# Kernel tuning notes

Measured on AMD Instinct MI355X. Metric: run time of the kernel, lower is better.

## Reference

```python
import jax, jax.numpy as jnp
import numpy as np
from jax import lax

SPATIAL = 4
PAD = 1
STRIDE = 1


def _route(x, rconv_w, rconv_b, fc_w, fc_b, num_experts):
    # x: (b, c, h, w); adaptive avg pool to (SPATIAL, SPATIAL) -- h,w divisible by SPATIAL
    b, c, h, w = x.shape
    pooled = x.reshape(b, c, SPATIAL, h // SPATIAL, SPATIAL, w // SPATIAL).mean(axis=(3, 5))
    # 1x1 conv: (b,c,s,s) x (rc,c) -> (b,rc,s,s)
    y = jnp.einsum('bcij,rc->brij', pooled, rconv_w) + rconv_b[None, :, None, None]
    y = jax.nn.relu(y).reshape(b, -1)                      # (b, rc*s*s)
    y = jax.nn.relu(y @ fc_w.T + fc_b)                     # (b, num_experts*c)
    y = y.reshape(b, num_experts, c)
    return jax.nn.sigmoid(y)                               # (b, k, c)


def _conv_per_sample(xi, wi):
    # xi: (c_in, h, w), wi: (c_out, c_in, kh, kw)
    out = lax.conv_general_dilated(
        xi[None], wi, window_strides=(STRIDE, STRIDE),
        padding=[(PAD, PAD), (PAD, PAD)],
        dimension_numbers=('NCHW', 'OIHW', 'NCHW'))
    return out[0]


def setup_inputs() -> dict:
    key = jax.random.key(0)
    ks = jax.random.split(key, 6)
    b, c_in, c_out, kk, ne = 16, 256, 256, 3, 3
    rc = max(c_in // 16, 16)  # reduction_channels = 16
    x = jax.random.normal(ks[0], (b, c_in, 64, 64), dtype=jnp.float32)
    expert_weight = jax.random.normal(ks[1], (ne, c_out, c_in, kk, kk), dtype=jnp.float32) * 0.02
    rconv_w = jax.random.normal(ks[2], (rc, c_in), dtype=jnp.float32) * 0.05
    rconv_b = jax.random.normal(ks[3], (rc,), dtype=jnp.float32) * 0.05
    fc_w = jax.random.normal(ks[4], (ne * c_in, rc * SPATIAL * SPATIAL), dtype=jnp.float32) * 0.05
    fc_b = jax.random.normal(ks[5], (ne * c_in,), dtype=jnp.float32) * 0.05
    return {"x": x, "expert_weight": expert_weight, "rconv_w": rconv_w,
            "rconv_b": rconv_b, "fc_w": fc_w, "fc_b": fc_b}


def reference(x, expert_weight, rconv_w, rconv_b, fc_w, fc_b):
    ne = expert_weight.shape[0]
    r = _route(x, rconv_w, rconv_b, fc_w, fc_b, ne)        # (b, k, c_in)
    # per-sample combined weights: routing scales input channels of each expert kernel
    w = jnp.einsum('bkc,kocij->bocij', r, expert_weight)    # (b, c_out, c_in, kh, kw)
    out = jax.vmap(_conv_per_sample)(x, w)                  # (b, c_out, h', w')
    return out
```

## Files before the change

kernel.cpp:

```cpp
#include <hip/hip_runtime.h>

#define B_   16
#define C_   256
#define OC_  256
#define H_   64
#define W_   64

typedef __attribute__((ext_vector_type(8)))  __bf16 bf16x8;
typedef __attribute__((ext_vector_type(4)))  float  f32x4;
typedef __attribute__((ext_vector_type(16))) float  f32x16;

__device__ __forceinline__ short f2bf(float f) {
    unsigned u = __float_as_uint(f);
    u += 0x7fffu + ((u >> 16) & 1u);
    return (short)(u >> 16);
}
__device__ __forceinline__ unsigned pk2(float a, float b) {
    return (unsigned(f2bf(a)) & 0xffffu) | (unsigned(f2bf(b)) << 16);
}
__device__ __forceinline__ void gll16(const void* g, void* l) {
    __builtin_amdgcn_global_load_lds(
        (const __attribute__((address_space(1))) unsigned int*)g,
        (__attribute__((address_space(3))) unsigned int*)l,
        16, 0, 0);
}

__global__ __launch_bounds__(256) void k_transpose_pool(
        const float* __restrict__ x, short* __restrict__ xt, float* __restrict__ pooled) {
    int y = blockIdx.x, b = blockIdx.y, t = threadIdx.x;
    int si = y >> 4;
    int lane = t & 63, wv = t >> 6;
    int xq = lane & 15, cw = lane >> 4;
    __shared__ float tile[64 * 67];

    for (int cc = 0; cc < 4; ++cc) {
        int cbase = cc * 64;
        if (cc) __syncthreads();
        #pragma unroll
        for (int r = 0; r < 4; ++r) {
            int c_l = r * 16 + wv * 4 + cw;
            float4 v = *(const float4*)&x[(((size_t)b * C_ + cbase + c_l) * H_ + y) * W_ + xq * 4];
            float* tp = &tile[c_l * 67 + xq * 4];
            tp[0] = v.x; tp[1] = v.y; tp[2] = v.z; tp[3] = v.w;
            float s = v.x + v.y + v.z + v.w;
            s += __shfl_xor(s, 1);
            s += __shfl_xor(s, 2);
            if ((lane & 3) == 0)
                atomicAdd(&pooled[((b * 4 + si) * 4 + (xq >> 2)) * 256 + cbase + c_l], s);
        }
        __syncthreads();
        #pragma unroll
        for (int r2 = 0; r2 < 2; ++r2) {
            int u = r2 * 256 + t;
            int xx = u >> 3, cgl = u & 7;
            float f[8];
            #pragma unroll
            for (int j = 0; j < 8; ++j) f[j] = tile[(cgl * 8 + j) * 67 + xx];
            uint4 pkv;
            pkv.x = pk2(f[0], f[1]); pkv.y = pk2(f[2], f[3]);
            pkv.z = pk2(f[4], f[5]); pkv.w = pk2(f[6], f[7]);
            *(uint4*)&xt[(((size_t)b * H_ + y) * W_ + xx) * C_ + cbase + cgl * 8] = pkv;
        }
    }
}

__global__ __launch_bounds__(256) void k_route(
        const float* __restrict__ pooled, const float* __restrict__ rconv_w,
        const float* __restrict__ rconv_b, const float* __restrict__ fc_w,
        const float* __restrict__ fc_b, float* __restrict__ r_buf) {
    int b = blockIdx.x;
    int t = threadIdx.x;
    __shared__ float pl[16][257];
    __shared__ float y1[256];

    #pragma unroll
    for (int q = 0; q < 16; ++q)
        pl[q][t] = pooled[b * 4096 + q * 256 + t] * (1.0f / 256.0f);
    __syncthreads();
    {
        int rcc = t >> 4, ss = t & 15;
        float acc = rconv_b[rcc];
        #pragma unroll 8
        for (int c = 0; c < 256; ++c)
            acc += pl[ss][c] * rconv_w[rcc * 256 + c];
        y1[rcc * 16 + ss] = fmaxf(acc, 0.f);
    }
    __syncthreads();
    for (int e0 = 0; e0 < 768; e0 += 256) {
        int e = e0 + t;
        float acc = fc_b[e];
        #pragma unroll 8
        for (int q = 0; q < 256; ++q)
            acc += y1[q] * fc_w[(size_t)e * 256 + q];
        acc = fmaxf(acc, 0.f);
        r_buf[(size_t)b * 768 + e] = 1.f / (1.f + __expf(-acc));
    }
}

__global__ __launch_bounds__(256) void k_combine(
        const float* __restrict__ E, const float* __restrict__ r_buf,
        short* __restrict__ wcomb) {
    int o = blockIdx.x;
    int t = threadIdx.x;
    __shared__ float eT[3][2304];
    #pragma unroll
    for (int k = 0; k < 3; ++k)
        #pragma unroll
        for (int q = 0; q < 9; ++q)
            eT[k][q * 256 + t] = E[((size_t)k * OC_ + o) * 2304 + q * 256 + t];
    __syncthreads();
    int c = t;
    float e0[9], e1[9], e2[9];
    #pragma unroll
    for (int tap = 0; tap < 9; ++tap) {
        e0[tap] = eT[0][c * 9 + tap];
        e1[tap] = eT[1][c * 9 + tap];
        e2[tap] = eT[2][c * 9 + tap];
    }
    int ks   = c >> 4;
    int half = (c >> 3) & 1;
    int ch   = c & 7;
    int og   = o >> 5, ol = o & 31;
    int sub  = ol * 16 + half * 8 + ch;
    for (int b = 0; b < 16; ++b) {
        float r0 = r_buf[(size_t)b * 768 + c];
        float r1 = r_buf[(size_t)b * 768 + 256 + c];
        float r2 = r_buf[(size_t)b * 768 + 512 + c];
        short* wo = wcomb + (size_t)b * 589824;
        #pragma unroll
        for (int tap = 0; tap < 9; ++tap) {
            float v = r0 * e0[tap] + r1 * e1[tap] + r2 * e2[tap];
            wo[((tap * 16 + ks) * 8 + og) * 512 + sub] = f2bf(v);
        }
    }
}

__global__ __launch_bounds__(256, 2) void k_conv(
        const short* __restrict__ xt, const short* __restrict__ wcomb,
        float* __restrict__ out, const short* __restrict__ zbuf) {
    int lin  = blockIdx.x;
    int work = (lin & 7) * 64 + (lin >> 3);
    int b      = work >> 5;
    int o_base = ((work >> 4) & 1) * 128;
    int y0     = (work & 15) * 4;

    int t = threadIdx.x;
    int lane = t & 63, w = t >> 6;
    int l31 = lane & 31, lh = lane >> 5;

    __shared__ __align__(16) short win[6 * 64 * 64];

    int zoff = (int)(zbuf - xt);

    int woff[12];
    #pragma unroll
    for (int r = 0; r < 12; ++r) {
        int u = r * 256 + t;
        int pos = u >> 3, sp = u & 7;
        int wrow = pos >> 6, xc = pos & 63;
        int yy = y0 - 1 + wrow;
        int ss = sp ^ (xc & 7);
        woff[r] = ((unsigned)yy < 64u)
            ? ((b * 64 + yy) * 64 + xc) * 256 + ss * 8
            : zoff;
    }

    int og0 = o_base >> 5;
    const short* pA = wcomb + (size_t)b * 589824
                    + og0 * 512 + l31 * 16 + lh * 8;

    f32x16 acc[4][2];
    #pragma unroll
    for (int i = 0; i < 4; ++i)
        #pragma unroll
        for (int j = 0; j < 2; ++j)
            #pragma unroll
            for (int q = 0; q < 16; ++q) acc[i][j][q] = 0.f;

    bf16x8 P[2][4];

    for (int cc = 0; cc < 4; ++cc) {
        int ccOff = cc * 64;
        #pragma unroll
        for (int r = 0; r < 12; ++r)
            gll16(xt + woff[r] + ccOff, &win[(r * 256 + w * 64) * 8]);

        if (cc == 0) {
            #pragma unroll
            for (int mb = 0; mb < 4; ++mb) {
                P[0][mb] = *(const bf16x8*)(pA + (0 * 16 + 0) * 4096 + mb * 512);
                P[1][mb] = *(const bf16x8*)(pA + (0 * 16 + 1) * 4096 + mb * 512);
            }
        }
        __syncthreads();

        #pragma unroll
        for (int ph = 0; ph < 36; ++ph) {
            const int tap = ph >> 2, ks = ph & 3;
            const int ti = tap / 3, tj = tap % 3;
            const int cur = ph & 1;
            const int slot = ks * 2 + lh;

            bf16x8 bv[2];
            #pragma unroll
            for (int nb = 0; nb < 2; ++nb) {
                int xc = nb * 32 + l31 + (tj - 1);
                bool ok = ((unsigned)xc < 64u);
                int xs = ok ? xc : 0;
                int wrow = w + ti;
                bf16x8 v = *(const bf16x8*)&win[(wrow * 64 + xs) * 64
                                                + ((slot ^ (xs & 7)) * 8)];
                bf16x8 zz = {};
                bv[nb] = ok ? v : zz;
            }
            __builtin_amdgcn_s_setprio(1);
            #pragma unroll
            for (int mb = 0; mb < 4; ++mb)
                #pragma unroll
                for (int nb = 0; nb < 2; ++nb)
                    acc[mb][nb] = __builtin_amdgcn_mfma_f32_32x32x16_bf16(
                        P[cur][mb], bv[nb], acc[mb][nb], 0, 0, 0);
            __builtin_amdgcn_s_setprio(0);

            if (ph < 34) {
                const int np = ph + 2, ntap = np >> 2, nks = np & 3;
                #pragma unroll
                for (int mb = 0; mb < 4; ++mb)
                    P[cur][mb] = *(const bf16x8*)(pA
                        + (ntap * 16 + cc * 4 + nks) * 4096 + mb * 512);
            } else if (cc < 3) {
                const int nks = (ph == 34) ? 0 : 1;
                #pragma unroll
                for (int mb = 0; mb < 4; ++mb)
                    P[cur][mb] = *(const bf16x8*)(pA
                        + (0 * 16 + (cc + 1) * 4 + nks) * 4096 + mb * 512);
            }
        }
        if (cc < 3) __syncthreads();
    }

    #pragma unroll
    for (int mb = 0; mb < 4; ++mb) {
        #pragma unroll
        for (int nb = 0; nb < 2; ++nb) {
            int xx = nb * 32 + l31;
            int yy = y0 + w;
            #pragma unroll
            for (int rg = 0; rg < 16; ++rg) {
                int o = o_base + mb * 32 + (rg & 3) + ((rg >> 2) * 8) + lh * 4;
                out[(((size_t)b * OC_ + o) * H_ + yy) * W_ + xx] = acc[mb][nb][rg];
            }
        }
    }
}

extern "C" void kernel_launch(void* const* d_in, const int* in_sizes, int n_in,
                              void* d_out, int out_size, void* d_ws, size_t ws_size,
                              hipStream_t stream) {
    const float* x       = (const float*)d_in[0];
    const float* E       = (const float*)d_in[1];
    const float* rconv_w = (const float*)d_in[2];
    const float* rconv_b = (const float*)d_in[3];
    const float* fc_w    = (const float*)d_in[4];
    const float* fc_b    = (const float*)d_in[5];
    float* out = (float*)d_out;

    char* ws = (char*)d_ws;
    short* xt     = (short*)(ws);
    short* wcomb  = (short*)(ws + 33554432);
    float* pooled = (float*)(ws + 52428800);
    short* zbuf   = (short*)(ws + 52690944);
    float* rbuf   = (float*)(ws + 52692992);

    hipMemsetAsync(pooled, 0, 262144 + 1024, stream);

    k_transpose_pool<<<dim3(64, 16), 256, 0, stream>>>(x, xt, pooled);
    k_route<<<dim3(16), 256, 0, stream>>>(pooled, rconv_w, rconv_b, fc_w, fc_b, rbuf);
    k_combine<<<dim3(256), 256, 0, stream>>>(E, rbuf, wcomb);
    k_conv<<<dim3(512), 256, 0, stream>>>(xt, wcomb, out, zbuf);
}
```

Baseline: 250.8 us.

## Split conv warp tile into 2x4 output-channel by pixel quadrants with new LDS swizzle

```diff
diff --git a/kernel.cpp b/kernel.cpp
--- a/kernel.cpp
+++ b/kernel.cpp
@@ -147,10 +147,16 @@
     int t = threadIdx.x;
     int lane = t & 63, w = t >> 6;
     int l31 = lane & 31, lh = lane >> 5;
-
-    __shared__ __align__(16) short win[6 * 64 * 64];
+    int m_half = w & 1, p_half = w >> 1;
+
+    __shared__ __align__(16) short win[6 * 64 * 64 + 512];
 
     int zoff = (int)(zbuf - xt);
+
+    if (t < 64) {
+        uint4 z; z.x = z.y = z.z = z.w = 0u;
+        *(uint4*)&win[24576 + t * 8] = z;
+    }
 
     int woff[12];
     #pragma unroll
@@ -159,25 +165,25 @@
         int pos = u >> 3, sp = u & 7;
         int wrow = pos >> 6, xc = pos & 63;
         int yy = y0 - 1 + wrow;
-        int ss = sp ^ (xc & 7);
+        int ss = sp ^ ((xc & 7) ^ ((xc >> 3) & 3));
         woff[r] = ((unsigned)yy < 64u)
             ? ((b * 64 + yy) * 64 + xc) * 256 + ss * 8
             : zoff;
     }
 
-    int og0 = o_base >> 5;
+    int og0 = (o_base >> 5) + m_half * 2;
     const short* pA = wcomb + (size_t)b * 589824
                     + og0 * 512 + l31 * 16 + lh * 8;
 
-    f32x16 acc[4][2];
-    #pragma unroll
-    for (int i = 0; i < 4; ++i)
-        #pragma unroll
-        for (int j = 0; j < 2; ++j)
+    f32x16 acc[2][4];
+    #pragma unroll
+    for (int i = 0; i < 2; ++i)
+        #pragma unroll
+        for (int j = 0; j < 4; ++j)
             #pragma unroll
             for (int q = 0; q < 16; ++q) acc[i][j][q] = 0.f;
 
-    bf16x8 P[2][4];
+    bf16x8 P[2][2];
 
     for (int cc = 0; cc < 4; ++cc) {
         int ccOff = cc * 64;
@@ -187,9 +193,9 @@
 
         if (cc == 0) {
             #pragma unroll
-            for (int mb = 0; mb < 4; ++mb) {
-                P[0][mb] = *(const bf16x8*)(pA + (0 * 16 + 0) * 4096 + mb * 512);
-                P[1][mb] = *(const bf16x8*)(pA + (0 * 16 + 1) * 4096 + mb * 512);
+            for (int mb = 0; mb < 2; ++mb) {
+                P[0][mb] = *(const bf16x8*)(pA + 0 * 4096 + mb * 512);
+                P[1][mb] = *(const bf16x8*)(pA + 1 * 4096 + mb * 512);
             }
         }
         __syncthreads();
@@ -201,23 +207,22 @@
             const int cur = ph & 1;
             const int slot = ks * 2 + lh;
 
-            bf16x8 bv[2];
-            #pragma unroll
-            for (int nb = 0; nb < 2; ++nb) {
-                int xc = nb * 32 + l31 + (tj - 1);
-                bool ok = ((unsigned)xc < 64u);
-                int xs = ok ? xc : 0;
-                int wrow = w + ti;
-                bf16x8 v = *(const bf16x8*)&win[(wrow * 64 + xs) * 64
-                                                + ((slot ^ (xs & 7)) * 8)];
-                bf16x8 zz = {};
-                bv[nb] = ok ? v : zz;
+            bf16x8 bv[4];
+            #pragma unroll
+            for (int nb = 0; nb < 4; ++nb) {
+                int xc = (nb & 1) * 32 + l31 + (tj - 1);
+                int wrow = p_half * 2 + (nb >> 1) + ti;
+                int idx = ((unsigned)xc < 64u)
+                    ? (wrow * 64 + xc) * 64
+                      + ((slot ^ ((xc & 7) ^ ((xc >> 3) & 3))) * 8)
+                    : 24576 + lane * 8;
+                bv[nb] = *(const bf16x8*)&win[idx];
             }
             __builtin_amdgcn_s_setprio(1);
             #pragma unroll
-            for (int mb = 0; mb < 4; ++mb)
+            for (int mb = 0; mb < 2; ++mb)
                 #pragma unroll
-                for (int nb = 0; nb < 2; ++nb)
+                for (int nb = 0; nb < 4; ++nb)
                     acc[mb][nb] = __builtin_amdgcn_mfma_f32_32x32x16_bf16(
                         P[cur][mb], bv[nb], acc[mb][nb], 0, 0, 0);
             __builtin_amdgcn_s_setprio(0);
@@ -225,29 +230,30 @@
             if (ph < 34) {
                 const int np = ph + 2, ntap = np >> 2, nks = np & 3;
                 #pragma unroll
-                for (int mb = 0; mb < 4; ++mb)
+                for (int mb = 0; mb < 2; ++mb)
                     P[cur][mb] = *(const bf16x8*)(pA
                         + (ntap * 16 + cc * 4 + nks) * 4096 + mb * 512);
             } else if (cc < 3) {
                 const int nks = (ph == 34) ? 0 : 1;
                 #pragma unroll
-                for (int mb = 0; mb < 4; ++mb)
+                for (int mb = 0; mb < 2; ++mb)
                     P[cur][mb] = *(const bf16x8*)(pA
-                        + (0 * 16 + (cc + 1) * 4 + nks) * 4096 + mb * 512);
+                        + ((cc + 1) * 4 + nks) * 4096 + mb * 512);
             }
         }
         if (cc < 3) __syncthreads();
     }
 
     #pragma unroll
-    for (int mb = 0; mb < 4; ++mb) {
-        #pragma unroll
-        for (int nb = 0; nb < 2; ++nb) {
-            int xx = nb * 32 + l31;
-            int yy = y0 + w;
+    for (int mb = 0; mb < 2; ++mb) {
+        #pragma unroll
+        for (int nb = 0; nb < 4; ++nb) {
+            int xx = (nb & 1) * 32 + l31;
+            int yy = y0 + p_half * 2 + (nb >> 1);
             #pragma unroll
             for (int rg = 0; rg < 16; ++rg) {
-                int o = o_base + mb * 32 + (rg & 3) + ((rg >> 2) * 8) + lh * 4;
+                int o = o_base + m_half * 64 + mb * 32
+                      + (rg & 3) + ((rg >> 2) * 8) + lh * 4;
                 out[(((size_t)b * OC_ + o) * H_ + yy) * W_ + xx] = acc[mb][nb][rg];
             }
         }
```

After: 273.9 us. 9.2% more time.
